# Optimization experiments

Measured on AMD Instinct MI355X. Metric: run time of the kernel, lower is better.

The kernel has to match this reference:

```python
import jax, jax.numpy as jnp
import numpy as np
from jax import lax

NEG_SLOPE = 0.2
BN_EPS = 1e-5


def _edges(n_nodes, n_total):
    # complete graph (no self loops) on the first n_nodes nodes, as in create_complete_graph,
    # plus PyG GATConv default add_self_loops over ALL n_total nodes.
    i = np.arange(n_nodes)
    src = np.repeat(i, n_nodes)
    dst = np.tile(i, n_nodes)
    keep = src != dst
    loops = np.arange(n_total)
    src = np.concatenate([src[keep], loops]).astype(np.int32)
    dst = np.concatenate([dst[keep], loops]).astype(np.int32)
    return jnp.asarray(src), jnp.asarray(dst)


def _bn_eval(x, g, b, m, v):
    # x: [B, C, H, W]; eval-mode batchnorm with running stats
    inv = g / jnp.sqrt(v + BN_EPS)
    return x * inv[None, :, None, None] + (b - m * inv)[None, :, None, None]


def _gat(x, W, a_src, a_dst, bias, src, dst, n_total):
    h = x @ W                      # [N, D_out]
    s = h @ a_src                  # [N] per-node source score
    d = h @ a_dst                  # [N] per-node dest score
    e = jax.nn.leaky_relu(s[src] + d[dst], NEG_SLOPE)          # [E]
    emax = jax.ops.segment_max(e, dst, num_segments=n_total)   # [N]
    ex = jnp.exp(e - emax[dst])
    denom = jax.ops.segment_sum(ex, dst, num_segments=n_total)
    alpha = ex / denom[dst]                                    # [E]
    out = jax.ops.segment_sum(alpha[:, None] * h[src], dst, num_segments=n_total)
    return out + bias


def setup_inputs() -> dict:
    key = jax.random.key(0)
    ks = jax.random.split(key, 12)
    B, H, W = 8, 64, 64

    def rn(k, shape, s):
        return jax.random.normal(k, shape, jnp.float32) * s

    return {
        "images": jax.random.normal(ks[0], (B, 3, H, W), jnp.float32),
        "conv1_w": rn(ks[1], (64, 3, 3, 3), 0.1), "conv1_b": jnp.zeros((64,), jnp.float32),
        "bn1_g": jnp.ones((64,), jnp.float32), "bn1_b": jnp.zeros((64,), jnp.float32),
        "bn1_m": jnp.zeros((64,), jnp.float32), "bn1_v": jnp.ones((64,), jnp.float32),
        "conv2_w": rn(ks[2], (128, 64, 3, 3), 0.05), "conv2_b": jnp.zeros((128,), jnp.float32),
        "bn2_g": jnp.ones((128,), jnp.float32), "bn2_b": jnp.zeros((128,), jnp.float32),
        "bn2_m": jnp.zeros((128,), jnp.float32), "bn2_v": jnp.ones((128,), jnp.float32),
        "gat1_w": rn(ks[3], (128, 256), 0.05), "gat1_asrc": rn(ks[4], (256,), 0.05),
        "gat1_adst": rn(ks[5], (256,), 0.05), "gat1_bias": jnp.zeros((256,), jnp.float32),
        "gat2_w": rn(ks[6], (256, 128), 0.05), "gat2_asrc": rn(ks[7], (128,), 0.05),
        "gat2_adst": rn(ks[8], (128,), 0.05), "gat2_bias": jnp.zeros((128,), jnp.float32),
        "out_w": rn(ks[9], (128, 10), 0.05), "out_b": jnp.zeros((10,), jnp.float32),
    }


def reference(images, conv1_w, conv1_b, bn1_g, bn1_b, bn1_m, bn1_v,
              conv2_w, conv2_b, bn2_g, bn2_b, bn2_m, bn2_v,
              gat1_w, gat1_asrc, gat1_adst, gat1_bias,
              gat2_w, gat2_asrc, gat2_adst, gat2_bias,
              out_w, out_b):
    dn = ("NCHW", "OIHW", "NCHW")
    x = lax.conv_general_dilated(images, conv1_w, (1, 1), "SAME", dimension_numbers=dn)
    x = x + conv1_b[None, :, None, None]
    x = jax.nn.relu(_bn_eval(x, bn1_g, bn1_b, bn1_m, bn1_v))
    x = lax.reduce_window(x, -jnp.inf, lax.max, (1, 1, 2, 2), (1, 1, 2, 2), "VALID")
    x = lax.conv_general_dilated(x, conv2_w, (1, 1), "SAME", dimension_numbers=dn)
    x = x + conv2_b[None, :, None, None]
    x = jax.nn.relu(_bn_eval(x, bn2_g, bn2_b, bn2_m, bn2_v))

    B = x.shape[0]
    n_nodes = x.shape[2] * x.shape[3]          # (H/2)*(W/2) = 1024
    x = x.reshape(B, 128, n_nodes).transpose(0, 2, 1).reshape(-1, 128)  # [B*n, 128]
    n_total = B * n_nodes
    src, dst = _edges(n_nodes, n_total)

    x = jax.nn.relu(_gat(x, gat1_w, gat1_asrc, gat1_adst, gat1_bias, src, dst, n_total))
    x = jax.nn.relu(_gat(x, gat2_w, gat2_asrc, gat2_adst, gat2_bias, src, dst, n_total))

    x = x.reshape(B, n_nodes, 128).mean(axis=1)   # global_mean_pool over each image's nodes
    logits = x @ out_w + out_b
    return jax.nn.log_softmax(logits, axis=1)
```

## Files before the change

### kernel.cpp

```cpp
#include <hip/hip_runtime.h>
#include <math.h>

#define BN_EPS 1e-5f
#define NEG_SLOPE 0.2f

__device__ __forceinline__ float relu_f(float x) { return x > 0.f ? x : 0.f; }
__device__ __forceinline__ float leaky_f(float z) { return z > 0.f ? z : NEG_SLOPE * z; }

__global__ void conv1_pool(const float* __restrict__ img, const float* __restrict__ w,
                           const float* __restrict__ cb, const float* __restrict__ g,
                           const float* __restrict__ bb, const float* __restrict__ m,
                           const float* __restrict__ vv, float* __restrict__ out)
{
    int blk = blockIdx.x;
    int q = blk & 3, cog = (blk >> 2) & 15, b = blk >> 6;
    int t = threadIdx.x;
    int x = t & 31, y = (q << 3) + (t >> 5);

    float acc[4][4] = {};
#pragma unroll
    for (int ci = 0; ci < 3; ++ci) {
        const float* ib = img + (b * 3 + ci) * 4096;
        float rv[4][4];
#pragma unroll
        for (int r = 0; r < 4; ++r) {
            int yy = 2 * y - 1 + r;
            bool yok = (unsigned)yy < 64u;
            const float* p = ib + yy * 64 + 2 * x;
            float2 c01 = yok ? *(const float2*)p : make_float2(0.f, 0.f);
            rv[r][1] = c01.x;
            rv[r][2] = c01.y;
            rv[r][0] = (yok && x > 0) ? p[-1] : 0.f;
            rv[r][3] = (yok && x < 31) ? p[2] : 0.f;
        }
#pragma unroll
        for (int j = 0; j < 4; ++j) {
            const float* wj = w + ((cog * 4 + j) * 3 + ci) * 9;
#pragma unroll
            for (int ky = 0; ky < 3; ++ky)
#pragma unroll
                for (int kx = 0; kx < 3; ++kx) {
                    float wvv = wj[ky * 3 + kx];
#pragma unroll
                    for (int py = 0; py < 2; ++py)
#pragma unroll
                        for (int px = 0; px < 2; ++px)
                            acc[j][py * 2 + px] += rv[py + ky][px + kx] * wvv;
                }
        }
    }
#pragma unroll
    for (int j = 0; j < 4; ++j) {
        int co = cog * 4 + j;
        float inv = g[co] / sqrtf(vv[co] + BN_EPS);
        float sh = cb[co] * inv + (bb[co] - m[co] * inv);
        float v0 = relu_f(acc[j][0] * inv + sh);
        float v1 = relu_f(acc[j][1] * inv + sh);
        float v2 = relu_f(acc[j][2] * inv + sh);
        float v3 = relu_f(acc[j][3] * inv + sh);
        out[((b * 64 + co) * 32 + y) * 32 + x] = fmaxf(fmaxf(v0, v1), fmaxf(v2, v3));
    }
}

__global__ void conv2_split(const float* __restrict__ in, const float* __restrict__ w,
                            float* __restrict__ pacc01, float* __restrict__ pacc23)
{
    int blk = blockIdx.x;
    int kz = blk & 3, half = (blk >> 2) & 1, cog = (blk >> 3) & 31, b = blk >> 8;
    int t = threadIdx.x;
    int x2p = (t & 15) * 2;
    int y = half * 16 + (t >> 4);
    bool xnz = x2p != 0;
    bool xhi = x2p == 30;
    const float* ibase = in + b * 64 * 1024 + kz * 16 * 1024;
    int xb = xnz ? x2p - 1 : 0;

    float acc[4][2] = {};

#pragma unroll 2
    for (int ci = 0; ci < 16; ++ci) {
        const float* cb2 = ibase + ci * 1024;
        float rc[3][4];
#pragma unroll
        for (int r = 0; r < 3; ++r) {
            int yy = y - 1 + r;
            bool yok = (unsigned)yy < 32u;
            const float* p = cb2 + yy * 32 + xb;
            float4 f = yok ? *(const float4*)p : make_float4(0.f, 0.f, 0.f, 0.f);
            rc[r][0] = xnz ? f.x : 0.f;
            rc[r][1] = xnz ? f.y : f.x;
            rc[r][2] = xnz ? f.z : f.y;
            float r3 = xnz ? f.w : f.z;
            rc[r][3] = xhi ? 0.f : r3;
        }
#pragma unroll
        for (int j = 0; j < 4; ++j) {
            const float* wj = w + ((cog * 4 + j) * 64 + kz * 16 + ci) * 9;
#pragma unroll
            for (int ky = 0; ky < 3; ++ky)
#pragma unroll
                for (int kx = 0; kx < 3; ++kx) {
                    float wvv = wj[ky * 3 + kx];
                    acc[j][0] += rc[ky][kx] * wvv;
                    acc[j][1] += rc[ky][kx + 1] * wvv;
                }
        }
    }

    float* pp = (kz & 2 ? pacc23 : pacc01) + (size_t)(kz & 1) * 1048576;
    int bid = b * 64 + cog * 2 + half;
    size_t base = ((size_t)bid * 256 + t) * 8;
    float4 s0 = {acc[0][0], acc[1][0], acc[2][0], acc[3][0]};
    float4 s1 = {acc[0][1], acc[1][1], acc[2][1], acc[3][1]};
    *(float4*)&pp[base] = s0;
    *(float4*)&pp[base + 4] = s1;
}

__global__ void conv2_combine(const float* __restrict__ p01, const float* __restrict__ p23,
                              const float* __restrict__ cb, const float* __restrict__ g,
                              const float* __restrict__ bb, const float* __restrict__ m,
                              const float* __restrict__ vv, float* __restrict__ x0)
{
    int gid = blockIdx.x * 256 + threadIdx.x;
    int t = gid & 255, bid = gid >> 8;
    int half = bid & 1, cog = (bid >> 1) & 31, b = bid >> 6;
    size_t off = (size_t)gid * 8;

    float4 s0 = {0.f, 0.f, 0.f, 0.f}, s1 = {0.f, 0.f, 0.f, 0.f};
    const float* pl0 = p01;
    const float* pl1 = p01 + 1048576;
    const float* pl2 = p23;
    const float* pl3 = p23 + 1048576;
#pragma unroll
    for (int kz = 0; kz < 4; ++kz) {
        const float* pp = kz == 0 ? pl0 : kz == 1 ? pl1 : kz == 2 ? pl2 : pl3;
        float4 u0 = *(const float4*)&pp[off];
        float4 u1 = *(const float4*)&pp[off + 4];
        s0.x += u0.x; s0.y += u0.y; s0.z += u0.z; s0.w += u0.w;
        s1.x += u1.x; s1.y += u1.y; s1.z += u1.z; s1.w += u1.w;
    }

    float4 gg = ((const float4*)g)[cog];
    float4 vvv = ((const float4*)vv)[cog];
    float4 bbb = ((const float4*)bb)[cog];
    float4 mm = ((const float4*)m)[cog];
    float4 cbb = ((const float4*)cb)[cog];
    float ix = gg.x / sqrtf(vvv.x + BN_EPS);
    float iy = gg.y / sqrtf(vvv.y + BN_EPS);
    float iz = gg.z / sqrtf(vvv.z + BN_EPS);
    float iw = gg.w / sqrtf(vvv.w + BN_EPS);
    float shx = cbb.x * ix + (bbb.x - mm.x * ix);
    float shy = cbb.y * iy + (bbb.y - mm.y * iy);
    float shz = cbb.z * iz + (bbb.z - mm.z * iz);
    float shw = cbb.w * iw + (bbb.w - mm.w * iw);

    float4 o0 = {relu_f(s0.x * ix + shx), relu_f(s0.y * iy + shy),
                 relu_f(s0.z * iz + shz), relu_f(s0.w * iw + shw)};
    float4 o1 = {relu_f(s1.x * ix + shx), relu_f(s1.y * iy + shy),
                 relu_f(s1.z * iz + shz), relu_f(s1.w * iw + shw)};

    int y = half * 16 + (t >> 4), x2p = (t & 15) * 2;
    int n0 = b * 1024 + y * 32 + x2p;
    *(float4*)&x0[(size_t)n0 * 128 + cog * 4] = o0;
    *(float4*)&x0[(size_t)(n0 + 1) * 128 + cog * 4] = o1;
}

template <int K, int N, bool SELF>
__global__ void gemm32(const float* __restrict__ A, const float* __restrict__ Ahi,
                       const float* __restrict__ abias,
                       const float* __restrict__ B, float* __restrict__ C)
{
    __shared__ float As[16][32];
    __shared__ float Bs[16][64];
    int t = threadIdx.x;
    int m0 = blockIdx.x * 32;
    int n0 = blockIdx.y * 64;
    int tx = t & 15, ty = t >> 4;
    int am = t >> 2, akq = (t & 3) * 4;
    bool hi = SELF && m0 >= 1024;
    const float* Ab = hi ? Ahi : A;
    float acc[4][4] = {};

    for (int k0 = 0; k0 < K; k0 += 16) {
        float4 av = *(const float4*)&Ab[(size_t)(m0 + am) * K + k0 + akq];
        if (hi) {
            float4 bz = *(const float4*)&abias[k0 + akq];
            av.x = relu_f(av.x + bz.x);
            av.y = relu_f(av.y + bz.y);
            av.z = relu_f(av.z + bz.z);
            av.w = relu_f(av.w + bz.w);
        }
        float4 bv0 = *(const float4*)&B[(size_t)(k0 + ty) * N + n0 + tx * 4];
        float4 bv1 = *(const float4*)&B[(size_t)(k0 + 8 + ty) * N + n0 + tx * 4];
        __syncthreads();
        As[akq + 0][am] = av.x;
        As[akq + 1][am] = av.y;
        As[akq + 2][am] = av.z;
        As[akq + 3][am] = av.w;
        *(float4*)&Bs[ty][tx * 4] = bv0;
        *(float4*)&Bs[ty + 8][tx * 4] = bv1;
        __syncthreads();
#pragma unroll
        for (int kk = 0; kk < 16; ++kk) {
            float4 a4 = *(const float4*)&As[kk][ty * 4];
            float4 b4 = *(const float4*)&Bs[kk][tx * 4];
            float aa[4] = {a4.x, a4.y, a4.z, a4.w};
            float bb4[4] = {b4.x, b4.y, b4.z, b4.w};
#pragma unroll
            for (int i = 0; i < 4; ++i)
#pragma unroll
                for (int j = 0; j < 4; ++j)
                    acc[i][j] += aa[i] * bb4[j];
        }
    }
#pragma unroll
    for (int i = 0; i < 4; ++i) {
        float4 o = {acc[i][0], acc[i][1], acc[i][2], acc[i][3]};
        *(float4*)&C[(size_t)(m0 + ty * 4 + i) * N + n0 + tx * 4] = o;
    }
}

__global__ void score_kernel(const float* __restrict__ h, const float* __restrict__ asrc,
                             const float* __restrict__ adst, float* __restrict__ s,
                             float* __restrict__ d, int D, int N)
{
    int gt = blockIdx.x * blockDim.x + threadIdx.x;
    int wave = gt >> 6, lane = gt & 63;
    if (wave >= N) return;
    const float* hp = h + (size_t)wave * D;
    float ss = 0.f, dd = 0.f;
    for (int c = lane; c < D; c += 64) {
        float hv = hp[c];
        ss += hv * asrc[c];
        dd += hv * adst[c];
    }
    for (int off = 32; off; off >>= 1) {
        ss += __shfl_down(ss, off);
        dd += __shfl_down(dd, off);
    }
    if (lane == 0) { s[wave] = ss; d[wave] = dd; }
}

template <int D, int KS>
__global__ void gat_agg_gemm(const float* __restrict__ h, const float* __restrict__ s,
                             const float* __restrict__ d, float* __restrict__ pacc,
                             float* __restrict__ pden)
{
    __shared__ float Ss[1024];
    __shared__ float As[16][32];
    __shared__ float Bs[16][64];
    __shared__ float red[2];
    __shared__ float part[16][32];

    const int CH = 1024 / KS;
    int t = threadIdx.x;
    int m0 = blockIdx.x * 32;
    int n0 = blockIdx.y * 64;
    int kz = blockIdx.z;
    int tx = t & 15, ty = t >> 4;
    int ug = t >> 3, vg4 = (t & 7) * 4;

    float4 sa = *(const float4*)&s[t * 8];
    float4 sb = *(const float4*)&s[t * 8 + 4];
    *(float4*)&Ss[t * 8] = sa;
    *(float4*)&Ss[t * 8 + 4] = sb;
    float lm = fmaxf(fmaxf(fmaxf(sa.x, sa.y), fmaxf(sa.z, sa.w)),
                     fmaxf(fmaxf(sb.x, sb.y), fmaxf(sb.z, sb.w)));
#pragma unroll
    for (int off = 1; off < 64; off <<= 1) lm = fmaxf(lm, __shfl_xor(lm, off));
    if ((t & 63) == 0) red[t >> 6] = lm;
    __syncthreads();
    float smax = fmaxf(red[0], red[1]);

    float4 dv = *(const float4*)&d[m0 + vg4];
    float4 mv = {leaky_f(smax + dv.x), leaky_f(smax + dv.y),
                 leaky_f(smax + dv.z), leaky_f(smax + dv.w)};
    float4 dsum = {0.f, 0.f, 0.f, 0.f};
    float acc[4][4] = {};

    for (int k0 = kz * CH; k0 < kz * CH + CH; k0 += 16) {
        float4 bv0 = *(const float4*)&h[(size_t)(k0 + ty) * D + n0 + tx * 4];
        float4 bv1 = *(const float4*)&h[(size_t)(k0 + 8 + ty) * D + n0 + tx * 4];
        float su = Ss[k0 + ug];
        float4 avv;
        avv.x = __expf(leaky_f(su + dv.x) - mv.x);
        avv.y = __expf(leaky_f(su + dv.y) - mv.y);
        avv.z = __expf(leaky_f(su + dv.z) - mv.z);
        avv.w = __expf(leaky_f(su + dv.w) - mv.w);
        dsum.x += avv.x; dsum.y += avv.y; dsum.z += avv.z; dsum.w += avv.w;
        __syncthreads();
        *(float4*)&As[ug][vg4] = avv;
        *(float4*)&Bs[ty][tx * 4] = bv0;
        *(float4*)&Bs[ty + 8][tx * 4] = bv1;
        __syncthreads();
#pragma unroll
        for (int kk = 0; kk < 16; ++kk) {
            float4 a4 = *(const float4*)&As[kk][ty * 4];
            float4 b4 = *(const float4*)&Bs[kk][tx * 4];
            float aa[4] = {a4.x, a4.y, a4.z, a4.w};
            float bb4[4] = {b4.x, b4.y, b4.z, b4.w};
#pragma unroll
            for (int i = 0; i < 4; ++i)
#pragma unroll
                for (int j = 0; j < 4; ++j)
                    acc[i][j] += aa[i] * bb4[j];
        }
    }

    __syncthreads();
    *(float4*)&part[ug][vg4] = dsum;
    __syncthreads();

#pragma unroll
    for (int i = 0; i < 4; ++i) {
        int r = ty * 4 + i;
        float4 o = {acc[i][0], acc[i][1], acc[i][2], acc[i][3]};
        *(float4*)&pacc[((size_t)kz * 1024 + m0 + r) * D + n0 + tx * 4] = o;
    }
    if (t < 32) {
        float den = 0.f;
#pragma unroll
        for (int u = 0; u < 16; ++u) den += part[u][t];
        pden[kz * 1024 + m0 + t] = den;
    }
}

template <int D, int KS>
__global__ void gat_combine(const float* __restrict__ pacc, const float* __restrict__ pden,
                            const float* __restrict__ bias, float* __restrict__ out)
{
    int idx = blockIdx.x * blockDim.x + threadIdx.x;
    if (idx >= 1024 * D / 4) return;
    int c4 = idx & (D / 4 - 1);
    int v = idx / (D / 4);
    float4 a = {0.f, 0.f, 0.f, 0.f};
    float den = 0.f;
#pragma unroll
    for (int ks = 0; ks < KS; ++ks) {
        float4 p = ((const float4*)pacc)[(size_t)(ks * 1024 + v) * (D / 4) + c4];
        a.x += p.x; a.y += p.y; a.z += p.z; a.w += p.w;
        den += pden[ks * 1024 + v];
    }
    float rd = 1.f / den;
    float4 bz = ((const float4*)bias)[c4];
    float4 o = {relu_f(a.x * rd + bz.x), relu_f(a.y * rd + bz.y),
                relu_f(a.z * rd + bz.z), relu_f(a.w * rd + bz.w)};
    ((float4*)out)[(size_t)v * (D / 4) + c4] = o;
}

__global__ void poolhead(const float* __restrict__ x2low, const float* __restrict__ h2,
                         const float* __restrict__ bias2, const float* __restrict__ ow,
                         const float* __restrict__ ob, float* __restrict__ out)
{
    __shared__ float red[256];
    __shared__ float pooled[128];
    __shared__ float logits[10];
    int b = blockIdx.x, t = threadIdx.x;
    int c = t & 127, hseg = t >> 7;
    float a0 = 0.f, a1 = 0.f, a2 = 0.f, a3 = 0.f;
    if (b == 0) {
        const float* p = x2low + ((size_t)hseg * 512) * 128 + c;
#pragma unroll 2
        for (int n = 0; n < 512; n += 4) {
            a0 += p[(size_t)n * 128];
            a1 += p[(size_t)(n + 1) * 128];
            a2 += p[(size_t)(n + 2) * 128];
            a3 += p[(size_t)(n + 3) * 128];
        }
    } else {
        float bz = bias2[c];
        const float* p = h2 + ((size_t)b * 1024 + hseg * 512) * 128 + c;
#pragma unroll 2
        for (int n = 0; n < 512; n += 4) {
            a0 += relu_f(p[(size_t)n * 128] + bz);
            a1 += relu_f(p[(size_t)(n + 1) * 128] + bz);
            a2 += relu_f(p[(size_t)(n + 2) * 128] + bz);
            a3 += relu_f(p[(size_t)(n + 3) * 128] + bz);
        }
    }
    red[t] = (a0 + a1) + (a2 + a3);
    __syncthreads();
    if (t < 128) pooled[t] = (red[t] + red[t + 128]) * (1.f / 1024.f);
    __syncthreads();
    if (t < 10) {
        float l = ob[t];
        for (int cc = 0; cc < 128; ++cc) l += pooled[cc] * ow[cc * 10 + t];
        logits[t] = l;
    }
    __syncthreads();
    if (t == 0) {
        float mx = logits[0];
        for (int j = 1; j < 10; ++j) mx = fmaxf(mx, logits[j]);
        float sum = 0.f;
        for (int j = 0; j < 10; ++j) sum += expf(logits[j] - mx);
        float lse = mx + logf(sum);
        for (int j = 0; j < 10; ++j) out[b * 10 + j] = logits[j] - lse;
    }
}

extern "C" void kernel_launch(void* const* d_in, const int* in_sizes, int n_in,
                              void* d_out, int out_size, void* d_ws, size_t ws_size,
                              hipStream_t stream)
{
    const float* images = (const float*)d_in[0];
    const float* c1w = (const float*)d_in[1];
    const float* c1b = (const float*)d_in[2];
    const float* bn1g = (const float*)d_in[3];
    const float* bn1b = (const float*)d_in[4];
    const float* bn1m = (const float*)d_in[5];
    const float* bn1v = (const float*)d_in[6];
    const float* c2w = (const float*)d_in[7];
    const float* c2b = (const float*)d_in[8];
    const float* bn2g = (const float*)d_in[9];
    const float* bn2b = (const float*)d_in[10];
    const float* bn2m = (const float*)d_in[11];
    const float* bn2v = (const float*)d_in[12];
    const float* g1w = (const float*)d_in[13];
    const float* g1as = (const float*)d_in[14];
    const float* g1ad = (const float*)d_in[15];
    const float* g1b = (const float*)d_in[16];
    const float* g2w = (const float*)d_in[17];
    const float* g2as = (const float*)d_in[18];
    const float* g2ad = (const float*)d_in[19];
    const float* g2b = (const float*)d_in[20];
    const float* ow = (const float*)d_in[21];
    const float* ob = (const float*)d_in[22];
    float* out = (float*)d_out;

    float* ws = (float*)d_ws;
    float* x1    = ws;
    float* bufc1 = ws + 2097152;
    float* h1    = ws + 2621440;
    float* x0    = ws + 4718592;
    float* h2    = ws + 5767168;
    float* s1    = ws + 6815744;
    float* d1    = ws + 6816768;
    float* s2    = ws + 6817792;
    float* d2    = ws + 6818816;
    float* pden1 = bufc1 + 16384;
    float* pden2 = bufc1 + 24576;
    float* pacc1 = x0;
    float* pacc2 = h1;
    float* x2    = x0;
    float* c2p01 = x1;
    float* c2p23 = h1;

    conv1_pool<<<512, 256, 0, stream>>>(images, c1w, c1b, bn1g, bn1b, bn1m, bn1v, bufc1);
    conv2_split<<<2048, 256, 0, stream>>>(bufc1, c2w, c2p01, c2p23);
    conv2_combine<<<512, 256, 0, stream>>>(c2p01, c2p23, c2b, bn2g, bn2b, bn2m, bn2v, x0);

    gemm32<128, 256, false><<<dim3(256, 4), 128, 0, stream>>>(x0, x0, nullptr, g1w, h1);
    score_kernel<<<256, 256, 0, stream>>>(h1, g1as, g1ad, s1, d1, 256, 1024);
    gat_agg_gemm<256, 8><<<dim3(32, 4, 8), 128, 0, stream>>>(h1, s1, d1, pacc1, pden1);
    gat_combine<256, 8><<<256, 256, 0, stream>>>(pacc1, pden1, g1b, x1);

    gemm32<256, 128, true><<<dim3(256, 2), 128, 0, stream>>>(x1, h1, g1b, g2w, h2);
    score_kernel<<<256, 256, 0, stream>>>(h2, g2as, g2ad, s2, d2, 128, 1024);
    gat_agg_gemm<128, 16><<<dim3(32, 2, 16), 128, 0, stream>>>(h2, s2, d2, pacc2, pden2);
    gat_combine<128, 16><<<128, 256, 0, stream>>>(pacc2, pden2, g2b, x2);

    poolhead<<<8, 256, 0, stream>>>(x2, h2, g2b, ow, ob, out);
}
```

Measured before the change: 227.1 us.

## Fuse all stages into one persistent cooperative kernel with grid syncs

Replaces the chain of separate kernel launches (conv1, conv2 split/combine, GEMMs, score, aggregation, combine, pool head) with a single cooperative persistent kernel. Blocks loop over the tiles of each stage and meet at grid.sync() between stages. The GEMM and aggregation tiles are reworked for 256-thread blocks with a 2x4 per-thread micro-tile. This removes per-launch overhead and inter-kernel gaps, but adds grid-wide barrier costs, and grid size is capped by occupancy.

```diff
diff --git a/kernel.cpp b/kernel.cpp
--- a/kernel.cpp
+++ b/kernel.cpp
@@ -1,5 +1,8 @@
 #include <hip/hip_runtime.h>
+#include <hip/hip_cooperative_groups.h>
 #include <math.h>
+
+namespace cg = cooperative_groups;
 
 #define BN_EPS 1e-5f
 #define NEG_SLOPE 0.2f
@@ -7,315 +10,98 @@
 __device__ __forceinline__ float relu_f(float x) { return x > 0.f ? x : 0.f; }
 __device__ __forceinline__ float leaky_f(float z) { return z > 0.f ? z : NEG_SLOPE * z; }
 
-__global__ void conv1_pool(const float* __restrict__ img, const float* __restrict__ w,
-                           const float* __restrict__ cb, const float* __restrict__ g,
-                           const float* __restrict__ bb, const float* __restrict__ m,
-                           const float* __restrict__ vv, float* __restrict__ out)
+template <int K, int N, bool SELF>
+__device__ void gemm_tile(const float* A, const float* Ahi, const float* abias,
+                          const float* B, float* C, int m0, int n0,
+                          float (*As)[33], float (*Bs)[64])
 {
-    int blk = blockIdx.x;
-    int q = blk & 3, cog = (blk >> 2) & 15, b = blk >> 6;
     int t = threadIdx.x;
-    int x = t & 31, y = (q << 3) + (t >> 5);
-
-    float acc[4][4] = {};
-#pragma unroll
-    for (int ci = 0; ci < 3; ++ci) {
-        const float* ib = img + (b * 3 + ci) * 4096;
-        float rv[4][4];
-#pragma unroll
-        for (int r = 0; r < 4; ++r) {
-            int yy = 2 * y - 1 + r;
-            bool yok = (unsigned)yy < 64u;
-            const float* p = ib + yy * 64 + 2 * x;
-            float2 c01 = yok ? *(const float2*)p : make_float2(0.f, 0.f);
-            rv[r][1] = c01.x;
-            rv[r][2] = c01.y;
-            rv[r][0] = (yok && x > 0) ? p[-1] : 0.f;
-            rv[r][3] = (yok && x < 31) ? p[2] : 0.f;
-        }
-#pragma unroll
-        for (int j = 0; j < 4; ++j) {
-            const float* wj = w + ((cog * 4 + j) * 3 + ci) * 9;
-#pragma unroll
-            for (int ky = 0; ky < 3; ++ky)
-#pragma unroll
-                for (int kx = 0; kx < 3; ++kx) {
-                    float wvv = wj[ky * 3 + kx];
-#pragma unroll
-                    for (int py = 0; py < 2; ++py)
-#pragma unroll
-                        for (int px = 0; px < 2; ++px)
-                            acc[j][py * 2 + px] += rv[py + ky][px + kx] * wvv;
-                }
-        }
-    }
-#pragma unroll
-    for (int j = 0; j < 4; ++j) {
-        int co = cog * 4 + j;
-        float inv = g[co] / sqrtf(vv[co] + BN_EPS);
-        float sh = cb[co] * inv + (bb[co] - m[co] * inv);
-        float v0 = relu_f(acc[j][0] * inv + sh);
-        float v1 = relu_f(acc[j][1] * inv + sh);
-        float v2 = relu_f(acc[j][2] * inv + sh);
-        float v3 = relu_f(acc[j][3] * inv + sh);
-        out[((b * 64 + co) * 32 + y) * 32 + x] = fmaxf(fmaxf(v0, v1), fmaxf(v2, v3));
-    }
-}
-
-__global__ void conv2_split(const float* __restrict__ in, const float* __restrict__ w,
-                            float* __restrict__ pacc01, float* __restrict__ pacc23)
-{
-    int blk = blockIdx.x;
-    int kz = blk & 3, half = (blk >> 2) & 1, cog = (blk >> 3) & 31, b = blk >> 8;
-    int t = threadIdx.x;
-    int x2p = (t & 15) * 2;
-    int y = half * 16 + (t >> 4);
-    bool xnz = x2p != 0;
-    bool xhi = x2p == 30;
-    const float* ibase = in + b * 64 * 1024 + kz * 16 * 1024;
-    int xb = xnz ? x2p - 1 : 0;
-
-    float acc[4][2] = {};
-
-#pragma unroll 2
-    for (int ci = 0; ci < 16; ++ci) {
-        const float* cb2 = ibase + ci * 1024;
-        float rc[3][4];
-#pragma unroll
-        for (int r = 0; r < 3; ++r) {
-            int yy = y - 1 + r;
-            bool yok = (unsigned)yy < 32u;
-            const float* p = cb2 + yy * 32 + xb;
-            float4 f = yok ? *(const float4*)p : make_float4(0.f, 0.f, 0.f, 0.f);
-            rc[r][0] = xnz ? f.x : 0.f;
-            rc[r][1] = xnz ? f.y : f.x;
-            rc[r][2] = xnz ? f.z : f.y;
-            float r3 = xnz ? f.w : f.z;
-            rc[r][3] = xhi ? 0.f : r3;
-        }
-#pragma unroll
-        for (int j = 0; j < 4; ++j) {
-            const float* wj = w + ((cog * 4 + j) * 64 + kz * 16 + ci) * 9;
-#pragma unroll
-            for (int ky = 0; ky < 3; ++ky)
-#pragma unroll
-                for (int kx = 0; kx < 3; ++kx) {
-                    float wvv = wj[ky * 3 + kx];
-                    acc[j][0] += rc[ky][kx] * wvv;
-                    acc[j][1] += rc[ky][kx + 1] * wvv;
-                }
-        }
-    }
-
-    float* pp = (kz & 2 ? pacc23 : pacc01) + (size_t)(kz & 1) * 1048576;
-    int bid = b * 64 + cog * 2 + half;
-    size_t base = ((size_t)bid * 256 + t) * 8;
-    float4 s0 = {acc[0][0], acc[1][0], acc[2][0], acc[3][0]};
-    float4 s1 = {acc[0][1], acc[1][1], acc[2][1], acc[3][1]};
-    *(float4*)&pp[base] = s0;
-    *(float4*)&pp[base + 4] = s1;
-}
-
-__global__ void conv2_combine(const float* __restrict__ p01, const float* __restrict__ p23,
-                              const float* __restrict__ cb, const float* __restrict__ g,
-                              const float* __restrict__ bb, const float* __restrict__ m,
-                              const float* __restrict__ vv, float* __restrict__ x0)
-{
-    int gid = blockIdx.x * 256 + threadIdx.x;
-    int t = gid & 255, bid = gid >> 8;
-    int half = bid & 1, cog = (bid >> 1) & 31, b = bid >> 6;
-    size_t off = (size_t)gid * 8;
-
-    float4 s0 = {0.f, 0.f, 0.f, 0.f}, s1 = {0.f, 0.f, 0.f, 0.f};
-    const float* pl0 = p01;
-    const float* pl1 = p01 + 1048576;
-    const float* pl2 = p23;
-    const float* pl3 = p23 + 1048576;
-#pragma unroll
-    for (int kz = 0; kz < 4; ++kz) {
-        const float* pp = kz == 0 ? pl0 : kz == 1 ? pl1 : kz == 2 ? pl2 : pl3;
-        float4 u0 = *(const float4*)&pp[off];
-        float4 u1 = *(const float4*)&pp[off + 4];
-        s0.x += u0.x; s0.y += u0.y; s0.z += u0.z; s0.w += u0.w;
-        s1.x += u1.x; s1.y += u1.y; s1.z += u1.z; s1.w += u1.w;
-    }
-
-    float4 gg = ((const float4*)g)[cog];
-    float4 vvv = ((const float4*)vv)[cog];
-    float4 bbb = ((const float4*)bb)[cog];
-    float4 mm = ((const float4*)m)[cog];
-    float4 cbb = ((const float4*)cb)[cog];
-    float ix = gg.x / sqrtf(vvv.x + BN_EPS);
-    float iy = gg.y / sqrtf(vvv.y + BN_EPS);
-    float iz = gg.z / sqrtf(vvv.z + BN_EPS);
-    float iw = gg.w / sqrtf(vvv.w + BN_EPS);
-    float shx = cbb.x * ix + (bbb.x - mm.x * ix);
-    float shy = cbb.y * iy + (bbb.y - mm.y * iy);
-    float shz = cbb.z * iz + (bbb.z - mm.z * iz);
-    float shw = cbb.w * iw + (bbb.w - mm.w * iw);
-
-    float4 o0 = {relu_f(s0.x * ix + shx), relu_f(s0.y * iy + shy),
-                 relu_f(s0.z * iz + shz), relu_f(s0.w * iw + shw)};
-    float4 o1 = {relu_f(s1.x * ix + shx), relu_f(s1.y * iy + shy),
-                 relu_f(s1.z * iz + shz), relu_f(s1.w * iw + shw)};
-
-    int y = half * 16 + (t >> 4), x2p = (t & 15) * 2;
-    int n0 = b * 1024 + y * 32 + x2p;
-    *(float4*)&x0[(size_t)n0 * 128 + cog * 4] = o0;
-    *(float4*)&x0[(size_t)(n0 + 1) * 128 + cog * 4] = o1;
-}
-
-template <int K, int N, bool SELF>
-__global__ void gemm32(const float* __restrict__ A, const float* __restrict__ Ahi,
-                       const float* __restrict__ abias,
-                       const float* __restrict__ B, float* __restrict__ C)
-{
-    __shared__ float As[16][32];
-    __shared__ float Bs[16][64];
-    int t = threadIdx.x;
-    int m0 = blockIdx.x * 32;
-    int n0 = blockIdx.y * 64;
     int tx = t & 15, ty = t >> 4;
-    int am = t >> 2, akq = (t & 3) * 4;
+    int am = t >> 3, ak2 = (t & 7) * 2;
     bool hi = SELF && m0 >= 1024;
     const float* Ab = hi ? Ahi : A;
-    float acc[4][4] = {};
-
+    float acc[2][4] = {};
     for (int k0 = 0; k0 < K; k0 += 16) {
-        float4 av = *(const float4*)&Ab[(size_t)(m0 + am) * K + k0 + akq];
+        float2 av = *(const float2*)&Ab[(size_t)(m0 + am) * K + k0 + ak2];
         if (hi) {
-            float4 bz = *(const float4*)&abias[k0 + akq];
-            av.x = relu_f(av.x + bz.x);
-            av.y = relu_f(av.y + bz.y);
-            av.z = relu_f(av.z + bz.z);
-            av.w = relu_f(av.w + bz.w);
-        }
-        float4 bv0 = *(const float4*)&B[(size_t)(k0 + ty) * N + n0 + tx * 4];
-        float4 bv1 = *(const float4*)&B[(size_t)(k0 + 8 + ty) * N + n0 + tx * 4];
-        __syncthreads();
-        As[akq + 0][am] = av.x;
-        As[akq + 1][am] = av.y;
-        As[akq + 2][am] = av.z;
-        As[akq + 3][am] = av.w;
-        *(float4*)&Bs[ty][tx * 4] = bv0;
-        *(float4*)&Bs[ty + 8][tx * 4] = bv1;
+            av.x = relu_f(av.x + abias[k0 + ak2]);
+            av.y = relu_f(av.y + abias[k0 + ak2 + 1]);
+        }
+        float4 bv = *(const float4*)&B[(size_t)(k0 + ty) * N + n0 + tx * 4];
+        __syncthreads();
+        As[ak2][am] = av.x;
+        As[ak2 + 1][am] = av.y;
+        *(float4*)&Bs[ty][tx * 4] = bv;
         __syncthreads();
 #pragma unroll
         for (int kk = 0; kk < 16; ++kk) {
-            float4 a4 = *(const float4*)&As[kk][ty * 4];
+            float a0 = As[kk][ty * 2], a1 = As[kk][ty * 2 + 1];
             float4 b4 = *(const float4*)&Bs[kk][tx * 4];
-            float aa[4] = {a4.x, a4.y, a4.z, a4.w};
-            float bb4[4] = {b4.x, b4.y, b4.z, b4.w};
-#pragma unroll
-            for (int i = 0; i < 4; ++i)
-#pragma unroll
-                for (int j = 0; j < 4; ++j)
-                    acc[i][j] += aa[i] * bb4[j];
-        }
-    }
-#pragma unroll
-    for (int i = 0; i < 4; ++i) {
+            acc[0][0] += a0 * b4.x; acc[0][1] += a0 * b4.y;
+            acc[0][2] += a0 * b4.z; acc[0][3] += a0 * b4.w;
+            acc[1][0] += a1 * b4.x; acc[1][1] += a1 * b4.y;
+            acc[1][2] += a1 * b4.z; acc[1][3] += a1 * b4.w;
+        }
+    }
+#pragma unroll
+    for (int i = 0; i < 2; ++i) {
         float4 o = {acc[i][0], acc[i][1], acc[i][2], acc[i][3]};
-        *(float4*)&C[(size_t)(m0 + ty * 4 + i) * N + n0 + tx * 4] = o;
+        *(float4*)&C[(size_t)(m0 + ty * 2 + i) * N + n0 + tx * 4] = o;
     }
 }
 
-__global__ void score_kernel(const float* __restrict__ h, const float* __restrict__ asrc,
-                             const float* __restrict__ adst, float* __restrict__ s,
-                             float* __restrict__ d, int D, int N)
+template <int D, int KS>
+__device__ void agg_tile(const float* h, const float* s, const float* d,
+                         float* pacc, float* pden, int m0, int n0, int kz,
+                         float* Ss, float (*As)[33], float (*Bs)[64],
+                         float* red, float (*part)[32])
 {
-    int gt = blockIdx.x * blockDim.x + threadIdx.x;
-    int wave = gt >> 6, lane = gt & 63;
-    if (wave >= N) return;
-    const float* hp = h + (size_t)wave * D;
-    float ss = 0.f, dd = 0.f;
-    for (int c = lane; c < D; c += 64) {
-        float hv = hp[c];
-        ss += hv * asrc[c];
-        dd += hv * adst[c];
-    }
-    for (int off = 32; off; off >>= 1) {
-        ss += __shfl_down(ss, off);
-        dd += __shfl_down(dd, off);
-    }
-    if (lane == 0) { s[wave] = ss; d[wave] = dd; }
-}
-
-template <int D, int KS>
-__global__ void gat_agg_gemm(const float* __restrict__ h, const float* __restrict__ s,
-                             const float* __restrict__ d, float* __restrict__ pacc,
-                             float* __restrict__ pden)
-{
-    __shared__ float Ss[1024];
-    __shared__ float As[16][32];
-    __shared__ float Bs[16][64];
-    __shared__ float red[2];
-    __shared__ float part[16][32];
-
-    const int CH = 1024 / KS;
     int t = threadIdx.x;
-    int m0 = blockIdx.x * 32;
-    int n0 = blockIdx.y * 64;
-    int kz = blockIdx.z;
-    int tx = t & 15, ty = t >> 4;
-    int ug = t >> 3, vg4 = (t & 7) * 4;
-
-    float4 sa = *(const float4*)&s[t * 8];
-    float4 sb = *(const float4*)&s[t * 8 + 4];
-    *(float4*)&Ss[t * 8] = sa;
-    *(float4*)&Ss[t * 8 + 4] = sb;
-    float lm = fmaxf(fmaxf(fmaxf(sa.x, sa.y), fmaxf(sa.z, sa.w)),
-                     fmaxf(fmaxf(sb.x, sb.y), fmaxf(sb.z, sb.w)));
+    float4 sa = *(const float4*)&s[t * 4];
+    *(float4*)&Ss[t * 4] = sa;
+    float lm = fmaxf(fmaxf(sa.x, sa.y), fmaxf(sa.z, sa.w));
 #pragma unroll
     for (int off = 1; off < 64; off <<= 1) lm = fmaxf(lm, __shfl_xor(lm, off));
     if ((t & 63) == 0) red[t >> 6] = lm;
     __syncthreads();
-    float smax = fmaxf(red[0], red[1]);
-
-    float4 dv = *(const float4*)&d[m0 + vg4];
-    float4 mv = {leaky_f(smax + dv.x), leaky_f(smax + dv.y),
-                 leaky_f(smax + dv.z), leaky_f(smax + dv.w)};
-    float4 dsum = {0.f, 0.f, 0.f, 0.f};
-    float acc[4][4] = {};
-
+    float smax = fmaxf(fmaxf(red[0], red[1]), fmaxf(red[2], red[3]));
+
+    int tx = t & 15, ty = t >> 4;
+    int vg2 = tx * 2;
+    float dv0 = d[m0 + vg2], dv1 = d[m0 + vg2 + 1];
+    float mv0 = leaky_f(smax + dv0), mv1 = leaky_f(smax + dv1);
+    float ds0 = 0.f, ds1 = 0.f;
+    float acc[2][4] = {};
+    const int CH = 1024 / KS;
     for (int k0 = kz * CH; k0 < kz * CH + CH; k0 += 16) {
-        float4 bv0 = *(const float4*)&h[(size_t)(k0 + ty) * D + n0 + tx * 4];
-        float4 bv1 = *(const float4*)&h[(size_t)(k0 + 8 + ty) * D + n0 + tx * 4];
-        float su = Ss[k0 + ug];
-        float4 avv;
-        avv.x = __expf(leaky_f(su + dv.x) - mv.x);
-        avv.y = __expf(leaky_f(su + dv.y) - mv.y);
-        avv.z = __expf(leaky_f(su + dv.z) - mv.z);
-        avv.w = __expf(leaky_f(su + dv.w) - mv.w);
-        dsum.x += avv.x; dsum.y += avv.y; dsum.z += avv.z; dsum.w += avv.w;
-        __syncthreads();
-        *(float4*)&As[ug][vg4] = avv;
-        *(float4*)&Bs[ty][tx * 4] = bv0;
-        *(float4*)&Bs[ty + 8][tx * 4] = bv1;
+        float4 bv = *(const float4*)&h[(size_t)(k0 + ty) * D + n0 + tx * 4];
+        float su = Ss[k0 + ty];
+        float a0 = __expf(leaky_f(su + dv0) - mv0);
+        float a1 = __expf(leaky_f(su + dv1) - mv1);
+        ds0 += a0; ds1 += a1;
+        __syncthreads();
+        As[ty][vg2] = a0;
+        As[ty][vg2 + 1] = a1;
+        *(float4*)&Bs[ty][tx * 4] = bv;
         __syncthreads();
 #pragma unroll
         for (int kk = 0; kk < 16; ++kk) {
-            float4 a4 = *(const float4*)&As[kk][ty * 4];
+            float a0m = As[kk][ty * 2], a1m = As[kk][ty * 2 + 1];
             float4 b4 = *(const float4*)&Bs[kk][tx * 4];
-            float aa[4] = {a4.x, a4.y, a4.z, a4.w};
-            float bb4[4] = {b4.x, b4.y, b4.z, b4.w};
-#pragma unroll
-            for (int i = 0; i < 4; ++i)
-#pragma unroll
-                for (int j = 0; j < 4; ++j)
-                    acc[i][j] += aa[i] * bb4[j];
-        }
-    }
-
+            acc[0][0] += a0m * b4.x; acc[0][1] += a0m * b4.y;
+            acc[0][2] += a0m * b4.z; acc[0][3] += a0m * b4.w;
+            acc[1][0] += a1m * b4.x; acc[1][1] += a1m * b4.y;
+            acc[1][2] += a1m * b4.z; acc[1][3] += a1m * b4.w;
+        }
+    }
     __syncthreads();
-    *(float4*)&part[ug][vg4] = dsum;
+    part[ty][vg2] = ds0;
+    part[ty][vg2 + 1] = ds1;
     __syncthreads();
-
-#pragma unroll
-    for (int i = 0; i < 4; ++i) {
-        int r = ty * 4 + i;
+#pragma unroll
+    for (int i = 0; i < 2; ++i) {
         float4 o = {acc[i][0], acc[i][1], acc[i][2], acc[i][3]};
-        *(float4*)&pacc[((size_t)kz * 1024 + m0 + r) * D + n0 + tx * 4] = o;
+        *(float4*)&pacc[((size_t)kz * 1024 + m0 + ty * 2 + i) * D + n0 + tx * 4] = o;
     }
     if (t < 32) {
         float den = 0.f;
@@ -325,76 +111,320 @@
     }
 }
 
-template <int D, int KS>
-__global__ void gat_combine(const float* __restrict__ pacc, const float* __restrict__ pden,
-                            const float* __restrict__ bias, float* __restrict__ out)
+__global__ __launch_bounds__(256, 4) void fused_all(
+    const float* __restrict__ img, const float* __restrict__ c1w, const float* __restrict__ c1b,
+    const float* __restrict__ bn1g, const float* __restrict__ bn1b,
+    const float* __restrict__ bn1m, const float* __restrict__ bn1v,
+    const float* __restrict__ c2w, const float* __restrict__ c2b,
+    const float* __restrict__ bn2g, const float* __restrict__ bn2b,
+    const float* __restrict__ bn2m, const float* __restrict__ bn2v,
+    const float* __restrict__ g1w, const float* __restrict__ g1as,
+    const float* __restrict__ g1ad, const float* __restrict__ g1b,
+    const float* __restrict__ g2w, const float* __restrict__ g2as,
+    const float* __restrict__ g2ad, const float* __restrict__ g2b,
+    const float* __restrict__ ow, const float* __restrict__ ob,
+    float* ws, float* __restrict__ out)
 {
-    int idx = blockIdx.x * blockDim.x + threadIdx.x;
-    if (idx >= 1024 * D / 4) return;
-    int c4 = idx & (D / 4 - 1);
-    int v = idx / (D / 4);
-    float4 a = {0.f, 0.f, 0.f, 0.f};
-    float den = 0.f;
-#pragma unroll
-    for (int ks = 0; ks < KS; ++ks) {
-        float4 p = ((const float4*)pacc)[(size_t)(ks * 1024 + v) * (D / 4) + c4];
-        a.x += p.x; a.y += p.y; a.z += p.z; a.w += p.w;
-        den += pden[ks * 1024 + v];
-    }
-    float rd = 1.f / den;
-    float4 bz = ((const float4*)bias)[c4];
-    float4 o = {relu_f(a.x * rd + bz.x), relu_f(a.y * rd + bz.y),
-                relu_f(a.z * rd + bz.z), relu_f(a.w * rd + bz.w)};
-    ((float4*)out)[(size_t)v * (D / 4) + c4] = o;
-}
-
-__global__ void poolhead(const float* __restrict__ x2low, const float* __restrict__ h2,
-                         const float* __restrict__ bias2, const float* __restrict__ ow,
-                         const float* __restrict__ ob, float* __restrict__ out)
-{
-    __shared__ float red[256];
-    __shared__ float pooled[128];
-    __shared__ float logits[10];
-    int b = blockIdx.x, t = threadIdx.x;
-    int c = t & 127, hseg = t >> 7;
-    float a0 = 0.f, a1 = 0.f, a2 = 0.f, a3 = 0.f;
-    if (b == 0) {
-        const float* p = x2low + ((size_t)hseg * 512) * 128 + c;
+    __shared__ float Ss[1024];
+    __shared__ float As[16][33];
+    __shared__ float Bs[16][64];
+    __shared__ float red[4];
+    __shared__ float part[16][32];
+
+    const int r = blockIdx.x;
+    const int t = threadIdx.x;
+    const int G = gridDim.x;
+    cg::grid_group grid = cg::this_grid();
+
+    float* x1    = ws;
+    float* bufc1 = ws + 2097152;
+    float* h1    = ws + 2621440;
+    float* x0    = ws + 4718592;
+    float* h2    = ws + 5767168;
+    float* s1    = ws + 6815744;
+    float* d1    = ws + 6816768;
+    float* s2    = ws + 6817792;
+    float* d2    = ws + 6818816;
+    float* pden1 = bufc1 + 16384;
+    float* pden2 = bufc1 + 24576;
+    float* pacc1 = x0;
+    float* pacc2 = h1;
+    float* x2    = x0;
+    float* c2p   = x1;
+
+    for (int vb = r; vb < 512; vb += G) {
+        int q = vb & 3, cog = (vb >> 2) & 15, b = vb >> 6;
+        int x = t & 31, y = (q << 3) + (t >> 5);
+        float acc[4][4] = {};
+#pragma unroll
+        for (int ci = 0; ci < 3; ++ci) {
+            const float* ib = img + (b * 3 + ci) * 4096;
+            float rv[4][4];
+#pragma unroll
+            for (int rr = 0; rr < 4; ++rr) {
+                int yy = 2 * y - 1 + rr;
+                bool yok = (unsigned)yy < 64u;
+                const float* p = ib + yy * 64 + 2 * x;
+                float2 c01 = yok ? *(const float2*)p : make_float2(0.f, 0.f);
+                rv[rr][1] = c01.x;
+                rv[rr][2] = c01.y;
+                rv[rr][0] = (yok && x > 0) ? p[-1] : 0.f;
+                rv[rr][3] = (yok && x < 31) ? p[2] : 0.f;
+            }
+#pragma unroll
+            for (int j = 0; j < 4; ++j) {
+                const float* wj = c1w + ((cog * 4 + j) * 3 + ci) * 9;
+#pragma unroll
+                for (int ky = 0; ky < 3; ++ky)
+#pragma unroll
+                    for (int kx = 0; kx < 3; ++kx) {
+                        float wvv = wj[ky * 3 + kx];
+#pragma unroll
+                        for (int py = 0; py < 2; ++py)
+#pragma unroll
+                            for (int px = 0; px < 2; ++px)
+                                acc[j][py * 2 + px] += rv[py + ky][px + kx] * wvv;
+                    }
+            }
+        }
+#pragma unroll
+        for (int j = 0; j < 4; ++j) {
+            int co = cog * 4 + j;
+            float inv = bn1g[co] / sqrtf(bn1v[co] + BN_EPS);
+            float sh = c1b[co] * inv + (bn1b[co] - bn1m[co] * inv);
+            float v0 = relu_f(acc[j][0] * inv + sh);
+            float v1 = relu_f(acc[j][1] * inv + sh);
+            float v2 = relu_f(acc[j][2] * inv + sh);
+            float v3 = relu_f(acc[j][3] * inv + sh);
+            bufc1[((b * 64 + co) * 32 + y) * 32 + x] = fmaxf(fmaxf(v0, v1), fmaxf(v2, v3));
+        }
+    }
+    grid.sync();
+
+    for (int vb = r; vb < 1024; vb += G) {
+        int kz = vb & 1, half = (vb >> 1) & 1, cog = (vb >> 2) & 31, b = vb >> 7;
+        int x2p = (t & 15) * 2;
+        int y = half * 16 + (t >> 4);
+        bool xnz = x2p != 0;
+        bool xhi = x2p == 30;
+        const float* ibase = bufc1 + b * 65536 + kz * 32768;
+        int xb = xnz ? x2p - 1 : 0;
+        float acc[4][2] = {};
 #pragma unroll 2
-        for (int n = 0; n < 512; n += 4) {
-            a0 += p[(size_t)n * 128];
-            a1 += p[(size_t)(n + 1) * 128];
-            a2 += p[(size_t)(n + 2) * 128];
-            a3 += p[(size_t)(n + 3) * 128];
-        }
-    } else {
-        float bz = bias2[c];
-        const float* p = h2 + ((size_t)b * 1024 + hseg * 512) * 128 + c;
+        for (int ci = 0; ci < 32; ++ci) {
+            const float* cbp = ibase + ci * 1024;
+            float rc[3][4];
+#pragma unroll
+            for (int rr = 0; rr < 3; ++rr) {
+                int yy = y - 1 + rr;
+                bool yok = (unsigned)yy < 32u;
+                const float* p = cbp + yy * 32 + xb;
+                float4 f = yok ? *(const float4*)p : make_float4(0.f, 0.f, 0.f, 0.f);
+                rc[rr][0] = xnz ? f.x : 0.f;
+                rc[rr][1] = xnz ? f.y : f.x;
+                rc[rr][2] = xnz ? f.z : f.y;
+                float r3 = xnz ? f.w : f.z;
+                rc[rr][3] = xhi ? 0.f : r3;
+            }
+#pragma unroll
+            for (int j = 0; j < 4; ++j) {
+                const float* wj = c2w + ((cog * 4 + j) * 64 + kz * 32 + ci) * 9;
+#pragma unroll
+                for (int ky = 0; ky < 3; ++ky)
+#pragma unroll
+                    for (int kx = 0; kx < 3; ++kx) {
+                        float wvv = wj[ky * 3 + kx];
+                        acc[j][0] += rc[ky][kx] * wvv;
+                        acc[j][1] += rc[ky][kx + 1] * wvv;
+                    }
+            }
+        }
+        float* pp = c2p + (size_t)kz * 1048576;
+        int bid = b * 64 + cog * 2 + half;
+        size_t base = ((size_t)bid * 256 + t) * 8;
+        float4 s0 = {acc[0][0], acc[1][0], acc[2][0], acc[3][0]};
+        float4 s1v = {acc[0][1], acc[1][1], acc[2][1], acc[3][1]};
+        *(float4*)&pp[base] = s0;
+        *(float4*)&pp[base + 4] = s1v;
+    }
+    grid.sync();
+
+    for (int vb = r; vb < 512; vb += G) {
+        int bid = vb;
+        int half = bid & 1, cog = (bid >> 1) & 31, b = bid >> 6;
+        size_t off = ((size_t)bid * 256 + t) * 8;
+        float4 u0 = *(const float4*)&c2p[off];
+        float4 u1 = *(const float4*)&c2p[off + 4];
+        float4 w0 = *(const float4*)&c2p[1048576 + off];
+        float4 w1 = *(const float4*)&c2p[1048576 + off + 4];
+        float sx = u0.x + w0.x, sy = u0.y + w0.y, sz = u0.z + w0.z, sw = u0.w + w0.w;
+        float qx = u1.x + w1.x, qy = u1.y + w1.y, qz = u1.z + w1.z, qw = u1.w + w1.w;
+
+        float4 gg = ((const float4*)bn2g)[cog];
+        float4 vvv = ((const float4*)bn2v)[cog];
+        float4 bbb = ((const float4*)bn2b)[cog];
+        float4 mm = ((const float4*)bn2m)[cog];
+        float4 cbb = ((const float4*)c2b)[cog];
+        float ix = gg.x / sqrtf(vvv.x + BN_EPS);
+        float iy = gg.y / sqrtf(vvv.y + BN_EPS);
+        float iz = gg.z / sqrtf(vvv.z + BN_EPS);
+        float iw = gg.w / sqrtf(vvv.w + BN_EPS);
+        float shx = cbb.x * ix + (bbb.x - mm.x * ix);
+        float shy = cbb.y * iy + (bbb.y - mm.y * iy);
+        float shz = cbb.z * iz + (bbb.z - mm.z * iz);
+        float shw = cbb.w * iw + (bbb.w - mm.w * iw);
+
+        float4 o0 = {relu_f(sx * ix + shx), relu_f(sy * iy + shy),
+                     relu_f(sz * iz + shz), relu_f(sw * iw + shw)};
+        float4 o1 = {relu_f(qx * ix + shx), relu_f(qy * iy + shy),
+                     relu_f(qz * iz + shz), relu_f(qw * iw + shw)};
+        int y = half * 16 + (t >> 4), x2p = (t & 15) * 2;
+        int n0 = b * 1024 + y * 32 + x2p;
+        *(float4*)&x0[(size_t)n0 * 128 + cog * 4] = o0;
+        *(float4*)&x0[(size_t)(n0 + 1) * 128 + cog * 4] = o1;
+    }
+    grid.sync();
+
+    for (int vb = r; vb < 1024; vb += G)
+        gemm_tile<128, 256, false>(x0, x0, nullptr, g1w, h1, (vb >> 2) * 32, (vb & 3) * 64, As, Bs);
+    grid.sync();
+
+    for (int wv = r * 4 + (t >> 6); wv < 1024; wv += G * 4) {
+        int lane = t & 63;
+        const float* hp = h1 + (size_t)wv * 256;
+        float ss = 0.f, dd = 0.f;
+#pragma unroll
+        for (int c0 = 0; c0 < 256; c0 += 64) {
+            float hv = hp[c0 + lane];
+            ss += hv * g1as[c0 + lane];
+            dd += hv * g1ad[c0 + lane];
+        }
+        for (int off = 32; off; off >>= 1) {
+            ss += __shfl_down(ss, off);
+            dd += __shfl_down(dd, off);
+        }
+        if (lane == 0) { s1[wv] = ss; d1[wv] = dd; }
+    }
+    grid.sync();
+
+    for (int vb = r; vb < 1024; vb += G)
+        agg_tile<256, 8>(h1, s1, d1, pacc1, pden1,
+                         (vb >> 5) * 32, ((vb >> 3) & 3) * 64, vb & 7,
+                         Ss, As, Bs, red, part);
+    grid.sync();
+
+    for (int vb = r; vb < 256; vb += G) {
+        int idx = (vb << 8) + t;
+        int c4 = idx & 63, v = idx >> 6;
+        float4 a = {0.f, 0.f, 0.f, 0.f};
+        float den = 0.f;
+#pragma unroll
+        for (int ks = 0; ks < 8; ++ks) {
+            float4 p = ((const float4*)pacc1)[(size_t)(ks * 1024 + v) * 64 + c4];
+            a.x += p.x; a.y += p.y; a.z += p.z; a.w += p.w;
+            den += pden1[ks * 1024 + v];
+        }
+        float rd = 1.f / den;
+        float4 bz = ((const float4*)g1b)[c4];
+        float4 o = {relu_f(a.x * rd + bz.x), relu_f(a.y * rd + bz.y),
+                    relu_f(a.z * rd + bz.z), relu_f(a.w * rd + bz.w)};
+        ((float4*)x1)[(size_t)v * 64 + c4] = o;
+    }
+    grid.sync();
+
+    for (int vb = r; vb < 512; vb += G)
+        gemm_tile<256, 128, true>(x1, h1, g1b, g2w, h2, (vb >> 1) * 32, (vb & 1) * 64, As, Bs);
+    grid.sync();
+
+    for (int wv = r * 4 + (t >> 6); wv < 1024; wv += G * 4) {
+        int lane = t & 63;
+        const float* hp = h2 + (size_t)wv * 128;
+        float ss = 0.f, dd = 0.f;
+#pragma unroll
+        for (int c0 = 0; c0 < 128; c0 += 64) {
+            float hv = hp[c0 + lane];
+            ss += hv * g2as[c0 + lane];
+            dd += hv * g2ad[c0 + lane];
+        }
+        for (int off = 32; off; off >>= 1) {
+            ss += __shfl_down(ss, off);
+            dd += __shfl_down(dd, off);
+        }
+        if (lane == 0) { s2[wv] = ss; d2[wv] = dd; }
+    }
+    grid.sync();
+
+    for (int vb = r; vb < 1024; vb += G)
+        agg_tile<128, 16>(h2, s2, d2, pacc2, pden2,
+                          (vb >> 5) * 32, ((vb >> 4) & 1) * 64, vb & 15,
+                          Ss, As, Bs, red, part);
+    grid.sync();
+
+    for (int vb = r; vb < 128; vb += G) {
+        int idx = (vb << 8) + t;
+        int c4 = idx & 31, v = idx >> 5;
+        float4 a = {0.f, 0.f, 0.f, 0.f};
+        float den = 0.f;
+#pragma unroll
+        for (int ks = 0; ks < 16; ++ks) {
+            float4 p = ((const float4*)pacc2)[(size_t)(ks * 1024 + v) * 32 + c4];
+            a.x += p.x; a.y += p.y; a.z += p.z; a.w += p.w;
+            den += pden2[ks * 1024 + v];
+        }
+        float rd = 1.f / den;
+        float4 bz = ((const float4*)g2b)[c4];
+        float4 o = {relu_f(a.x * rd + bz.x), relu_f(a.y * rd + bz.y),
+                    relu_f(a.z * rd + bz.z), relu_f(a.w * rd + bz.w)};
+        ((float4*)x2)[(size_t)v * 32 + c4] = o;
+    }
+    grid.sync();
+
+    for (int vb = r; vb < 8; vb += G) {
+        int b = vb;
+        float* red256 = Ss;
+        float* pooled = Ss + 256;
+        float* logits = Ss + 384;
+        int c = t & 127, hseg = t >> 7;
+        float a0 = 0.f, a1 = 0.f, a2 = 0.f, a3 = 0.f;
+        if (b == 0) {
+            const float* p = x2 + ((size_t)hseg * 512) * 128 + c;
 #pragma unroll 2
-        for (int n = 0; n < 512; n += 4) {
-            a0 += relu_f(p[(size_t)n * 128] + bz);
-            a1 += relu_f(p[(size_t)(n + 1) * 128] + bz);
-            a2 += relu_f(p[(size_t)(n + 2) * 128] + bz);
-            a3 += relu_f(p[(size_t)(n + 3) * 128] + bz);
-        }
-    }
-    red[t] = (a0 + a1) + (a2 + a3);
-    __syncthreads();
-    if (t < 128) pooled[t] = (red[t] + red[t + 128]) * (1.f / 1024.f);
-    __syncthreads();
-    if (t < 10) {
-        float l = ob[t];
-        for (int cc = 0; cc < 128; ++cc) l += pooled[cc] * ow[cc * 10 + t];
-        logits[t] = l;
-    }
-    __syncthreads();
-    if (t == 0) {
-        float mx = logits[0];
-        for (int j = 1; j < 10; ++j) mx = fmaxf(mx, logits[j]);
-        float sum = 0.f;
-        for (int j = 0; j < 10; ++j) sum += expf(logits[j] - mx);
-        float lse = mx + logf(sum);
-        for (int j = 0; j < 10; ++j) out[b * 10 + j] = logits[j] - lse;
+            for (int n = 0; n < 512; n += 4) {
+                a0 += p[(size_t)n * 128];
+                a1 += p[(size_t)(n + 1) * 128];
+                a2 += p[(size_t)(n + 2) * 128];
+                a3 += p[(size_t)(n + 3) * 128];
+            }
+        } else {
+            float bz = g2b[c];
+            const float* p = h2 + ((size_t)b * 1024 + hseg * 512) * 128 + c;
+#pragma unroll 2
+            for (int n = 0; n < 512; n += 4) {
+                a0 += relu_f(p[(size_t)n * 128] + bz);
+                a1 += relu_f(p[(size_t)(n + 1) * 128] + bz);
+                a2 += relu_f(p[(size_t)(n + 2) * 128] + bz);
+                a3 += relu_f(p[(size_t)(n + 3) * 128] + bz);
+            }
+        }
+        red256[t] = (a0 + a1) + (a2 + a3);
+        __syncthreads();
+        if (t < 128) pooled[t] = (red256[t] + red256[t + 128]) * (1.f / 1024.f);
+        __syncthreads();
+        if (t < 10) {
+            float l = ob[t];
+            for (int cc = 0; cc < 128; ++cc) l += pooled[cc] * ow[cc * 10 + t];
+            logits[t] = l;
+        }
+        __syncthreads();
+        if (t == 0) {
+            float mx = logits[0];
+            for (int j = 1; j < 10; ++j) mx = fmaxf(mx, logits[j]);
+            float sum = 0.f;
+            for (int j = 0; j < 10; ++j) sum += expf(logits[j] - mx);
+            float lse = mx + logf(sum);
+            for (int j = 0; j < 10; ++j) out[b * 10 + j] = logits[j] - lse;
+        }
+        __syncthreads();
     }
 }
 
@@ -426,38 +456,29 @@
     const float* ow = (const float*)d_in[21];
     const float* ob = (const float*)d_in[22];
     float* out = (float*)d_out;
-
-    float* ws = (float*)d_ws;
-    float* x1    = ws;
-    float* bufc1 = ws + 2097152;
-    float* h1    = ws + 2621440;
-    float* x0    = ws + 4718592;
-    float* h2    = ws + 5767168;
-    float* s1    = ws + 6815744;
-    float* d1    = ws + 6816768;
-    float* s2    = ws + 6817792;
-    float* d2    = ws + 6818816;
-    float* pden1 = bufc1 + 16384;
-    float* pden2 = bufc1 + 24576;
-    float* pacc1 = x0;
-    float* pacc2 = h1;
-    float* x2    = x0;
-    float* c2p01 = x1;
-    float* c2p23 = h1;
-
-    conv1_pool<<<512, 256, 0, stream>>>(images, c1w, c1b, bn1g, bn1b, bn1m, bn1v, bufc1);
-    conv2_split<<<2048, 256, 0, stream>>>(bufc1, c2w, c2p01, c2p23);
-    conv2_combine<<<512, 256, 0, stream>>>(c2p01, c2p23, c2b, bn2g, bn2b, bn2m, bn2v, x0);
-
-    gemm32<128, 256, false><<<dim3(256, 4), 128, 0, stream>>>(x0, x0, nullptr, g1w, h1);
-    score_kernel<<<256, 256, 0, stream>>>(h1, g1as, g1ad, s1, d1, 256, 1024);
-    gat_agg_gemm<256, 8><<<dim3(32, 4, 8), 128, 0, stream>>>(h1, s1, d1, pacc1, pden1);
-    gat_combine<256, 8><<<256, 256, 0, stream>>>(pacc1, pden1, g1b, x1);
-
-    gemm32<256, 128, true><<<dim3(256, 2), 128, 0, stream>>>(x1, h1, g1b, g2w, h2);
-    score_kernel<<<256, 256, 0, stream>>>(h2, g2as, g2ad, s2, d2, 128, 1024);
-    gat_agg_gemm<128, 16><<<dim3(32, 2, 16), 128, 0, stream>>>(h2, s2, d2, pacc2, pden2);
-    gat_combine<128, 16><<<128, 256, 0, stream>>>(pacc2, pden2, g2b, x2);
-
-    poolhead<<<8, 256, 0, stream>>>(x2, h2, g2b, ow, ob, out);
+    float* wsf = (float*)d_ws;
+
+    static int nblk = 0;
+    if (nblk == 0) {
+        int per_cu = 0;
+        hipOccupancyMaxActiveBlocksPerMultiprocessor(&per_cu, fused_all, 256, 0);
+        hipDeviceProp_t prop;
+        int dev = 0;
+        hipGetDevice(&dev);
+        hipGetDeviceProperties(&prop, dev);
+        if (per_cu < 1) per_cu = 1;
+        long cap = (long)per_cu * prop.multiProcessorCount;
+        nblk = cap < 1024 ? (int)cap : 1024;
+    }
+
+    void* params[25];
+    params[0] = &images; params[1] = &c1w;  params[2] = &c1b;
+    params[3] = &bn1g;   params[4] = &bn1b; params[5] = &bn1m;  params[6] = &bn1v;
+    params[7] = &c2w;    params[8] = &c2b;
+    params[9] = &bn2g;   params[10] = &bn2b; params[11] = &bn2m; params[12] = &bn2v;
+    params[13] = &g1w;   params[14] = &g1as; params[15] = &g1ad; params[16] = &g1b;
+    params[17] = &g2w;   params[18] = &g2as; params[19] = &g2ad; params[20] = &g2b;
+    params[21] = &ow;    params[22] = &ob;   params[23] = &wsf;  params[24] = &out;
+
+    hipLaunchCooperativeKernel((void*)fused_all, dim3(nblk), dim3(256), params, 0, stream);
 }
```

Result: slower. 874.0 us (+284.8%).
